# Kernel optimization log

Measured on AMD Instinct MI355X. Metric: run time of the kernel, lower is better.

The kernel has to match this reference:

```python
import jax, jax.numpy as jnp
from jax import lax
import numpy as np


def _dilate3x3(img):
    # Faithful to torch: zero-pad by 1 (f.pad default), then 3x3 max over the
    # padded window (strel of ones => plain max, zeros from padding included).
    imgp = jnp.pad(img, ((0, 0), (0, 0), (1, 1), (1, 1)))
    return lax.reduce_window(imgp, -jnp.inf, lax.max,
                             (1, 1, 3, 3), (1, 1, 1, 1), 'VALID')


def setup_inputs() -> dict:
    key = jax.random.key(0)
    x = jax.random.normal(key, (32, 3, 512, 512), dtype=jnp.float32)
    return {"in_tensor": x, "n_pixels": 20}


def reference(in_tensor, n_pixels):
    # smoother = linspace(1, 0, n+1); smoother_diff = -diff => 1/n per step (linear)
    smoother = jnp.linspace(1.0, 0.0, n_pixels + 1)
    sdiff = (-jnp.diff(smoother)).astype(in_tensor.dtype)  # [n_pixels]

    def step(carry, w):
        out, img = carry
        out = out + w * img
        img = _dilate3x3(img)
        return (out, img), None

    init = (jnp.zeros_like(in_tensor), in_tensor)
    (out, _), _ = lax.scan(step, init, sdiff)
    return out
```

## Files before the change

### kernel.cpp

```cpp
#include <hip/hip_runtime.h>

#define IMG_W 512
#define IMG_H 512
#define TILE 88
#define HALO 20
#define NSTEP 19
#define RH 8
#define RW 8

__device__ __forceinline__ float max3f(float a, float b, float c) {
    return fmaxf(fmaxf(a, b), c);
}

__global__ __launch_bounds__(256, 2)
void blur_outwards_kernel(const float* __restrict__ x, float* __restrict__ out) {
    const int tid = threadIdx.x;
    const int tx = tid & 15;
    const int ty = tid >> 4;

    const int ch  = blockIdx.z;
    const int gx0 = (int)blockIdx.x * TILE - HALO;
    const int gy0 = (int)blockIdx.y * TILE - HALO;

    const float* __restrict__ xc = x + (size_t)ch * (IMG_W * IMG_H);
    float* __restrict__ oc = out + (size_t)ch * (IMG_W * IMG_H);

    const int rx = tx * RW;
    const int ry = ty * RH;
    const int gx = gx0 + rx;
    const int gy = gy0 + ry;

    float A[RH][RW];
    float acc[RH][RW];
    float rowm[RH], colm[RW];

    #pragma unroll
    for (int c = 0; c < RW; ++c) {
        int xx = gx + c;
        colm[c] = (xx >= 0 && xx < IMG_W) ? 1.f : 0.f;
    }
    #pragma unroll
    for (int r = 0; r < RH; ++r) {
        int yy = gy + r;
        rowm[r] = (yy >= 0 && yy < IMG_H) ? 1.f : 0.f;
    }

    #pragma unroll
    for (int r = 0; r < RH; ++r) {
        int yy = min(max(gy + r, 0), IMG_H - 1);
        const float* rp = xc + yy * IMG_W;
        #pragma unroll
        for (int c = 0; c < RW; ++c) {
            int xx = min(max(gx + c, 0), IMG_W - 1);
            float v = rp[xx] * (rowm[r] * colm[c]);
            A[r][c] = v;
            acc[r][c] = v;
        }
    }

    __shared__ __align__(16) float topH[2][16][16][RW];
    __shared__ __align__(16) float botH[2][16][16][RW];

    #pragma unroll 1
    for (int s = 0; s < NSTEP; ++s) {
        const int buf = s & 1;
        float hc[RW], h7[RW];
        {
            float left  = __shfl_up(A[0][RW-1], 1);
            float right = __shfl_down(A[0][0], 1);
            hc[0] = max3f(left, A[0][0], A[0][1]) * colm[0];
            #pragma unroll
            for (int c = 1; c < RW-1; ++c)
                hc[c] = max3f(A[0][c-1], A[0][c], A[0][c+1]) * colm[c];
            hc[RW-1] = max3f(A[0][RW-2], A[0][RW-1], right) * colm[RW-1];
        }
        {
            float left  = __shfl_up(A[RH-1][RW-1], 1);
            float right = __shfl_down(A[RH-1][0], 1);
            h7[0] = max3f(left, A[RH-1][0], A[RH-1][1]) * colm[0];
            #pragma unroll
            for (int c = 1; c < RW-1; ++c)
                h7[c] = max3f(A[RH-1][c-1], A[RH-1][c], A[RH-1][c+1]) * colm[c];
            h7[RW-1] = max3f(A[RH-1][RW-2], A[RH-1][RW-1], right) * colm[RW-1];
        }
        #pragma unroll
        for (int c = 0; c < RW; ++c) {
            topH[buf][ty][tx][c] = hc[c];
            botH[buf][ty][tx][c] = h7[c];
        }
        __syncthreads();
        float hm1[RW], hbot[RW];
        {
            const int tyu = ty > 0  ? ty - 1 : 0;
            const int tyd = ty < 15 ? ty + 1 : 15;
            #pragma unroll
            for (int c = 0; c < RW; ++c) {
                hm1[c]  = botH[buf][tyu][tx][c];
                hbot[c] = topH[buf][tyd][tx][c];
            }
        }
        #pragma unroll
        for (int r = 0; r < RH; ++r) {
            float hn[RW];
            if (r < RH-2) {
                float left  = __shfl_up(A[r+1][RW-1], 1);
                float right = __shfl_down(A[r+1][0], 1);
                hn[0] = max3f(left, A[r+1][0], A[r+1][1]) * colm[0];
                #pragma unroll
                for (int c = 1; c < RW-1; ++c)
                    hn[c] = max3f(A[r+1][c-1], A[r+1][c], A[r+1][c+1]) * colm[c];
                hn[RW-1] = max3f(A[r+1][RW-2], A[r+1][RW-1], right) * colm[RW-1];
            } else if (r == RH-2) {
                #pragma unroll
                for (int c = 0; c < RW; ++c) hn[c] = h7[c];
            } else {
                #pragma unroll
                for (int c = 0; c < RW; ++c) hn[c] = hbot[c];
            }
            #pragma unroll
            for (int c = 0; c < RW; ++c) {
                float v = max3f(hm1[c], hc[c], hn[c]) * rowm[r];
                A[r][c] = v;
                acc[r][c] += v;
            }
            #pragma unroll
            for (int c = 0; c < RW; ++c) { hm1[c] = hc[c]; hc[c] = hn[c]; }
        }
    }

    #pragma unroll
    for (int r = 0; r < RH; ++r) {
        const int rr = ry + r;
        const int yy = gy0 + rr;
        if (rr >= HALO && rr < HALO + TILE && yy < IMG_H) {
            #pragma unroll
            for (int c = 0; c < RW; ++c) {
                const int cc = rx + c;
                const int xx = gx0 + cc;
                if (cc >= HALO && cc < HALO + TILE && xx < IMG_W) {
                    oc[yy * IMG_W + xx] = 0.05f * acc[r][c];
                }
            }
        }
    }
}

extern "C" void kernel_launch(void* const* d_in, const int* in_sizes, int n_in,
                              void* d_out, int out_size, void* d_ws, size_t ws_size,
                              hipStream_t stream) {
    const float* x = (const float*)d_in[0];
    float* out = (float*)d_out;
    dim3 grid((IMG_W + TILE - 1) / TILE,
              (IMG_H + TILE - 1) / TILE,
              96);
    blur_outwards_kernel<<<grid, 256, 0, stream>>>(x, out);
}
```

Baseline: 346.4 us.

## Split interior/edge tile paths, use DPP lane shifts and vectorized LDS/global access

Templates the kernel body on whether a tile lies fully inside the image, so interior tiles skip the boundary masks, clamped loads and per-element store checks and use float4 global loads and stores. Replaces the shfl_up/down calls with DPP row-shift intrinsics and lays out the shared halo buffers as float4 for wider LDS accesses. The DPP row shifts only move data within 16-lane rows, which matches the 16-wide tx layout. Having two instantiations grows code size and may change register allocation.

Measured after the change: 309.1 us. 10.8% less time.

```diff
diff --git a/kernel.cpp b/kernel.cpp
--- a/kernel.cpp
+++ b/kernel.cpp
@@ -7,24 +7,42 @@
 #define NSTEP 19
 #define RH 8
 #define RW 8
+#define REG 128
 
 __device__ __forceinline__ float max3f(float a, float b, float c) {
     return fmaxf(fmaxf(a, b), c);
 }
 
-__global__ __launch_bounds__(256, 2)
-void blur_outwards_kernel(const float* __restrict__ x, float* __restrict__ out) {
-    const int tid = threadIdx.x;
-    const int tx = tid & 15;
-    const int ty = tid >> 4;
-
-    const int ch  = blockIdx.z;
-    const int gx0 = (int)blockIdx.x * TILE - HALO;
-    const int gy0 = (int)blockIdx.y * TILE - HALO;
-
-    const float* __restrict__ xc = x + (size_t)ch * (IMG_W * IMG_H);
-    float* __restrict__ oc = out + (size_t)ch * (IMG_W * IMG_H);
-
+__device__ __forceinline__ float dpp_shr1(float v) {
+    int i = __builtin_bit_cast(int, v);
+    i = __builtin_amdgcn_update_dpp(i, i, 0x111, 0xf, 0xf, false);
+    return __builtin_bit_cast(float, i);
+}
+__device__ __forceinline__ float dpp_shl1(float v) {
+    int i = __builtin_bit_cast(int, v);
+    i = __builtin_amdgcn_update_dpp(i, i, 0x101, 0xf, 0xf, false);
+    return __builtin_bit_cast(float, i);
+}
+
+template<bool MASKED>
+__device__ __forceinline__ void hrow(const float (&Ar)[RW], const float (&colm)[RW],
+                                     float (&h)[RW]) {
+    float hl = dpp_shr1(Ar[RW - 1]);
+    float hr = dpp_shl1(Ar[0]);
+    h[0] = max3f(hl, Ar[0], Ar[1]);
+    #pragma unroll
+    for (int c = 1; c < RW - 1; ++c) h[c] = max3f(Ar[c - 1], Ar[c], Ar[c + 1]);
+    h[RW - 1] = max3f(Ar[RW - 2], Ar[RW - 1], hr);
+    if (MASKED) {
+        #pragma unroll
+        for (int c = 0; c < RW; ++c) h[c] *= colm[c];
+    }
+}
+
+template<bool EDGE>
+__device__ __forceinline__ void body(const float* __restrict__ xc, float* __restrict__ oc,
+                                     int gx0, int gy0, int tx, int ty,
+                                     float4 (*topH4)[2][16][16], float4 (*botH4)[2][16][16]) {
     const int rx = tx * RW;
     const int ry = ty * RH;
     const int gx = gx0 + rx;
@@ -34,83 +52,73 @@
     float acc[RH][RW];
     float rowm[RH], colm[RW];
 
-    #pragma unroll
-    for (int c = 0; c < RW; ++c) {
-        int xx = gx + c;
-        colm[c] = (xx >= 0 && xx < IMG_W) ? 1.f : 0.f;
-    }
-    #pragma unroll
-    for (int r = 0; r < RH; ++r) {
-        int yy = gy + r;
-        rowm[r] = (yy >= 0 && yy < IMG_H) ? 1.f : 0.f;
-    }
-
-    #pragma unroll
-    for (int r = 0; r < RH; ++r) {
-        int yy = min(max(gy + r, 0), IMG_H - 1);
-        const float* rp = xc + yy * IMG_W;
+    if (EDGE) {
         #pragma unroll
         for (int c = 0; c < RW; ++c) {
-            int xx = min(max(gx + c, 0), IMG_W - 1);
-            float v = rp[xx] * (rowm[r] * colm[c]);
-            A[r][c] = v;
-            acc[r][c] = v;
-        }
-    }
-
-    __shared__ __align__(16) float topH[2][16][16][RW];
-    __shared__ __align__(16) float botH[2][16][16][RW];
+            int xx = gx + c;
+            colm[c] = (xx >= 0 && xx < IMG_W) ? 1.f : 0.f;
+        }
+        #pragma unroll
+        for (int r = 0; r < RH; ++r) {
+            int yy = gy + r;
+            rowm[r] = (yy >= 0 && yy < IMG_H) ? 1.f : 0.f;
+        }
+        #pragma unroll
+        for (int r = 0; r < RH; ++r) {
+            int yy = min(max(gy + r, 0), IMG_H - 1);
+            const float* rp = xc + (size_t)yy * IMG_W;
+            #pragma unroll
+            for (int c = 0; c < RW; ++c) {
+                int xx = min(max(gx + c, 0), IMG_W - 1);
+                float v = rp[xx] * (rowm[r] * colm[c]);
+                A[r][c] = v;
+                acc[r][c] = v;
+            }
+        }
+    } else {
+        #pragma unroll
+        for (int c = 0; c < RW; ++c) colm[c] = 1.f;
+        #pragma unroll
+        for (int r = 0; r < RH; ++r) rowm[r] = 1.f;
+        #pragma unroll
+        for (int r = 0; r < RH; ++r) {
+            const float4* rp = (const float4*)(xc + (size_t)(gy + r) * IMG_W + gx);
+            float4 v0 = rp[0], v1 = rp[1];
+            A[r][0] = v0.x; A[r][1] = v0.y; A[r][2] = v0.z; A[r][3] = v0.w;
+            A[r][4] = v1.x; A[r][5] = v1.y; A[r][6] = v1.z; A[r][7] = v1.w;
+            #pragma unroll
+            for (int c = 0; c < RW; ++c) acc[r][c] = A[r][c];
+        }
+    }
 
     #pragma unroll 1
     for (int s = 0; s < NSTEP; ++s) {
         const int buf = s & 1;
         float hc[RW], h7[RW];
-        {
-            float left  = __shfl_up(A[0][RW-1], 1);
-            float right = __shfl_down(A[0][0], 1);
-            hc[0] = max3f(left, A[0][0], A[0][1]) * colm[0];
-            #pragma unroll
-            for (int c = 1; c < RW-1; ++c)
-                hc[c] = max3f(A[0][c-1], A[0][c], A[0][c+1]) * colm[c];
-            hc[RW-1] = max3f(A[0][RW-2], A[0][RW-1], right) * colm[RW-1];
-        }
-        {
-            float left  = __shfl_up(A[RH-1][RW-1], 1);
-            float right = __shfl_down(A[RH-1][0], 1);
-            h7[0] = max3f(left, A[RH-1][0], A[RH-1][1]) * colm[0];
-            #pragma unroll
-            for (int c = 1; c < RW-1; ++c)
-                h7[c] = max3f(A[RH-1][c-1], A[RH-1][c], A[RH-1][c+1]) * colm[c];
-            h7[RW-1] = max3f(A[RH-1][RW-2], A[RH-1][RW-1], right) * colm[RW-1];
-        }
-        #pragma unroll
-        for (int c = 0; c < RW; ++c) {
-            topH[buf][ty][tx][c] = hc[c];
-            botH[buf][ty][tx][c] = h7[c];
-        }
+        hrow<EDGE>(A[0], colm, hc);
+        hrow<EDGE>(A[RH - 1], colm, h7);
+        topH4[buf][0][ty][tx] = make_float4(hc[0], hc[1], hc[2], hc[3]);
+        topH4[buf][1][ty][tx] = make_float4(hc[4], hc[5], hc[6], hc[7]);
+        botH4[buf][0][ty][tx] = make_float4(h7[0], h7[1], h7[2], h7[3]);
+        botH4[buf][1][ty][tx] = make_float4(h7[4], h7[5], h7[6], h7[7]);
         __syncthreads();
+        const int tyu = ty > 0  ? ty - 1 : 0;
+        const int tyd = ty < 15 ? ty + 1 : 15;
         float hm1[RW], hbot[RW];
         {
-            const int tyu = ty > 0  ? ty - 1 : 0;
-            const int tyd = ty < 15 ? ty + 1 : 15;
-            #pragma unroll
-            for (int c = 0; c < RW; ++c) {
-                hm1[c]  = botH[buf][tyu][tx][c];
-                hbot[c] = topH[buf][tyd][tx][c];
-            }
+            float4 u0 = botH4[buf][0][tyu][tx], u1 = botH4[buf][1][tyu][tx];
+            float4 d0 = topH4[buf][0][tyd][tx], d1 = topH4[buf][1][tyd][tx];
+            hm1[0] = u0.x; hm1[1] = u0.y; hm1[2] = u0.z; hm1[3] = u0.w;
+            hm1[4] = u1.x; hm1[5] = u1.y; hm1[6] = u1.z; hm1[7] = u1.w;
+            hbot[0] = d0.x; hbot[1] = d0.y; hbot[2] = d0.z; hbot[3] = d0.w;
+            hbot[4] = d1.x; hbot[5] = d1.y; hbot[6] = d1.z; hbot[7] = d1.w;
         }
         #pragma unroll
         for (int r = 0; r < RH; ++r) {
             float hn[RW];
-            if (r < RH-2) {
-                float left  = __shfl_up(A[r+1][RW-1], 1);
-                float right = __shfl_down(A[r+1][0], 1);
-                hn[0] = max3f(left, A[r+1][0], A[r+1][1]) * colm[0];
-                #pragma unroll
-                for (int c = 1; c < RW-1; ++c)
-                    hn[c] = max3f(A[r+1][c-1], A[r+1][c], A[r+1][c+1]) * colm[c];
-                hn[RW-1] = max3f(A[r+1][RW-2], A[r+1][RW-1], right) * colm[RW-1];
-            } else if (r == RH-2) {
+            if (r < RH - 2) {
+                hrow<EDGE>(A[r + 1], colm, hn);
+            } else if (r == RH - 2) {
                 #pragma unroll
                 for (int c = 0; c < RW; ++c) hn[c] = h7[c];
             } else {
@@ -119,7 +127,8 @@
             }
             #pragma unroll
             for (int c = 0; c < RW; ++c) {
-                float v = max3f(hm1[c], hc[c], hn[c]) * rowm[r];
+                float v = max3f(hm1[c], hc[c], hn[c]);
+                if (EDGE) v *= rowm[r];
                 A[r][c] = v;
                 acc[r][c] += v;
             }
@@ -128,21 +137,64 @@
         }
     }
 
-    #pragma unroll
-    for (int r = 0; r < RH; ++r) {
-        const int rr = ry + r;
-        const int yy = gy0 + rr;
-        if (rr >= HALO && rr < HALO + TILE && yy < IMG_H) {
-            #pragma unroll
-            for (int c = 0; c < RW; ++c) {
-                const int cc = rx + c;
-                const int xx = gx0 + cc;
-                if (cc >= HALO && cc < HALO + TILE && xx < IMG_W) {
-                    oc[yy * IMG_W + xx] = 0.05f * acc[r][c];
+    if (EDGE) {
+        #pragma unroll
+        for (int r = 0; r < RH; ++r) {
+            const int rr = ry + r;
+            const int yy = gy0 + rr;
+            if (rr >= HALO && rr < HALO + TILE && yy < IMG_H) {
+                #pragma unroll
+                for (int c = 0; c < RW; ++c) {
+                    const int cc = rx + c;
+                    const int xx = gx0 + cc;
+                    if (cc >= HALO && cc < HALO + TILE && xx < IMG_W)
+                        oc[(size_t)yy * IMG_W + xx] = 0.05f * acc[r][c];
                 }
             }
         }
-    }
+    } else {
+        #pragma unroll
+        for (int r = 0; r < RH; ++r) {
+            const int rr = ry + r;
+            if (rr < HALO || rr >= HALO + TILE) continue;
+            const int yy = gy0 + rr;
+            float* rowp = oc + (size_t)yy * IMG_W + gx;
+            if (tx >= 3 && tx <= 12) {
+                ((float4*)rowp)[0] = make_float4(0.05f * acc[r][0], 0.05f * acc[r][1],
+                                                 0.05f * acc[r][2], 0.05f * acc[r][3]);
+                ((float4*)rowp)[1] = make_float4(0.05f * acc[r][4], 0.05f * acc[r][5],
+                                                 0.05f * acc[r][6], 0.05f * acc[r][7]);
+            } else if (tx == 2) {
+                ((float4*)rowp)[1] = make_float4(0.05f * acc[r][4], 0.05f * acc[r][5],
+                                                 0.05f * acc[r][6], 0.05f * acc[r][7]);
+            } else if (tx == 13) {
+                ((float4*)rowp)[0] = make_float4(0.05f * acc[r][0], 0.05f * acc[r][1],
+                                                 0.05f * acc[r][2], 0.05f * acc[r][3]);
+            }
+        }
+    }
+}
+
+__global__ __launch_bounds__(256, 2)
+void blur_outwards_kernel(const float* __restrict__ x, float* __restrict__ out) {
+    __shared__ float4 topH4[2][2][16][16];
+    __shared__ float4 botH4[2][2][16][16];
+
+    const int tid = threadIdx.x;
+    const int tx = tid & 15;
+    const int ty = tid >> 4;
+
+    const int ch  = blockIdx.z;
+    const int gx0 = (int)blockIdx.x * TILE - HALO;
+    const int gy0 = (int)blockIdx.y * TILE - HALO;
+
+    const float* __restrict__ xc = x + (size_t)ch * (IMG_W * IMG_H);
+    float* __restrict__ oc = out + (size_t)ch * (IMG_W * IMG_H);
+
+    const bool interior = (gx0 >= 0) && (gy0 >= 0) &&
+                          (gx0 + REG <= IMG_W) && (gy0 + REG <= IMG_H);
+    if (interior) body<false>(xc, oc, gx0, gy0, tx, ty, topH4, botH4);
+    else          body<true >(xc, oc, gx0, gy0, tx, ty, topH4, botH4);
 }
 
 extern "C" void kernel_launch(void* const* d_in, const int* in_sizes, int n_in,
```
